# Performance work log

Measured on AMD Instinct MI355X. Metric: run time of the kernel, lower is better.

Reference implementation:

```python
import jax, jax.numpy as jnp
import numpy as np

NUM_HEADS = 8
EMBED = 512
HEAD_DIM = EMBED // NUM_HEADS
B, S = 4, 2048


def setup_inputs() -> dict:
    key = jax.random.key(0)
    ks = jax.random.split(key, 8)
    sc = 0.02
    return {
        "values": jax.random.normal(ks[0], (B, S, EMBED), dtype=jnp.float32),
        "keys": jax.random.normal(ks[1], (B, S, EMBED), dtype=jnp.float32),
        "query": jax.random.normal(ks[2], (B, S, EMBED), dtype=jnp.float32),
        "Wv": jax.random.normal(ks[3], (HEAD_DIM, HEAD_DIM), dtype=jnp.float32) * sc,
        "Wk": jax.random.normal(ks[4], (HEAD_DIM, HEAD_DIM), dtype=jnp.float32) * sc,
        "Wq": jax.random.normal(ks[5], (HEAD_DIM, HEAD_DIM), dtype=jnp.float32) * sc,
        "Wo": jax.random.normal(ks[6], (EMBED, EMBED), dtype=jnp.float32) * sc,
        "bo": jnp.zeros((EMBED,), dtype=jnp.float32),
    }


def reference(values, keys, query, Wv, Wk, Wq, Wo, bo):
    b, s, _ = query.shape
    # split heads: [B, S, H, D]
    v = values.reshape(b, s, NUM_HEADS, HEAD_DIM)
    k = keys.reshape(b, s, NUM_HEADS, HEAD_DIM)
    q = query.reshape(b, s, NUM_HEADS, HEAD_DIM)
    # per-head linear (nn.Linear: x @ W.T), weights shared across heads
    v = jnp.einsum("bshd,ed->bshe", v, Wv)
    k = jnp.einsum("bshd,ed->bshe", k, Wk)
    q = jnp.einsum("bshd,ed->bshe", q, Wq)
    # energy: [B, H, Q, K]
    energy = jnp.einsum("bqhd,bkhd->bhqk", q, k)
    # NOTE: original scales by sqrt(embed_size), not sqrt(head_dim)
    attn = jax.nn.softmax(energy / jnp.sqrt(jnp.float32(EMBED)), axis=-1)
    out = jnp.einsum("bhqk,bkhd->bqhd", attn, v).reshape(b, s, EMBED)
    return out @ Wo.T + bo
```

## Files before the change

kernel.cpp:

```cpp
#include <hip/hip_runtime.h>

#define H 8
#define D 64
#define E 512
#define BATCH 4
#define SEQ 2048

typedef __bf16 bf16v8 __attribute__((ext_vector_type(8)));
typedef float f32v4 __attribute__((ext_vector_type(4)));
typedef unsigned int u32v4 __attribute__((ext_vector_type(4)));
typedef unsigned short u16v4 __attribute__((ext_vector_type(4)));

#define MFMA16(a,b,c) __builtin_amdgcn_mfma_f32_16x16x32_bf16(a,b,c,0,0,0)

#define AS1 __attribute__((address_space(1)))
#define AS3 __attribute__((address_space(3)))
#define GLDS16(g, l) __builtin_amdgcn_global_load_lds((const AS1 void*)(g), (AS3 void*)(l), 16, 0, 0)

static __device__ __forceinline__ unsigned short f2bf(float f) {
  unsigned u = __builtin_bit_cast(unsigned, f);
  u += 0x7fffu + ((u >> 16) & 1u);
  return (unsigned short)(u >> 16);
}

static __device__ __forceinline__ float exp2_hw(float x) {
#if __has_builtin(__builtin_amdgcn_exp2f)
  return __builtin_amdgcn_exp2f(x);
#else
  return exp2f(x);
#endif
}

static __device__ __forceinline__ bf16v8 lds16(const char* p) {
  return __builtin_bit_cast(bf16v8, *(const u32v4*)p);
}

static __device__ __forceinline__ unsigned cvtpk(float a, float b) {
  unsigned r;
  asm("v_cvt_pk_bf16_f32 %0, %1, %2" : "=v"(r) : "v"(a), "v"(b));
  return r;
}

__global__ void prep_all(const float* __restrict__ Wo, const float* __restrict__ Wv,
                         const float* __restrict__ Wq, const float* __restrict__ Wk,
                         const float* __restrict__ v, const float* __restrict__ keys,
                         unsigned short* __restrict__ Wo2, unsigned short* __restrict__ MT,
                         unsigned short* __restrict__ vT, unsigned short* __restrict__ kb) {
  __shared__ float tile[64][65];
  int bx = blockIdx.x;
  int t = threadIdx.x;
  if (bx < 1024) {
    int i = bx * 256 + t;
    int n = i >> 9, c = i & 511;
    int h = c >> 6, d = c & 63;
    float acc = 0.f;
    for (int e = 0; e < 64; ++e) acc += Wo[n*512 + h*64 + e] * Wv[e*64 + d];
    Wo2[n*512 + c] = f2bf(acc);
  } else if (bx < 1040) {
    int i = (bx - 1024) * 256 + t;
    int d2 = i >> 6, d1 = i & 63;
    float acc = 0.f;
    for (int e = 0; e < 64; ++e) acc += Wq[e*64 + d1] * Wk[e*64 + d2];
    MT[d2*64 + d1] = f2bf(acc * 0.04419417382415922f);
  } else {
    int flat = bx - 1040;
    int bh = flat >> 5, sc = flat & 31;
    int b = bh >> 3, h = bh & 7;
    {
      const float* kp = keys + (size_t)flat * 4096;
      unsigned short* ko = kb + (size_t)flat * 4096;
      #pragma unroll
      for (int i = 0; i < 4; ++i) {
        f32v4 x = *(const f32v4*)(kp + (i*256 + t)*4);
        u16v4 o = { f2bf(x[0]), f2bf(x[1]), f2bf(x[2]), f2bf(x[3]) };
        *(u16v4*)(ko + (i*256 + t)*4) = o;
      }
    }
    #pragma unroll
    for (int i = 0; i < 4; ++i) {
      int idx = i*256 + t; int si = idx >> 4, fc = (idx & 15)*4;
      *(f32v4*)&tile[si][fc] =
          *(const f32v4*)(v + (size_t)(b*SEQ + sc*64 + si)*E + h*64 + fc);
    }
    __syncthreads();
    #pragma unroll
    for (int i = 0; i < 4; ++i) {
      int idx = i*256 + t; int d = idx >> 4, s4 = (idx & 15)*4;
      u16v4 o = { f2bf(tile[s4+0][d]), f2bf(tile[s4+1][d]),
                  f2bf(tile[s4+2][d]), f2bf(tile[s4+3][d]) };
      *(u16v4*)(vT + (size_t)(bh*64 + d)*SEQ + sc*64 + s4) = o;
    }
  }
}

__global__ __launch_bounds__(256, 4) void attn(const float* __restrict__ query,
                                               const unsigned short* __restrict__ MT,
                                               const unsigned short* __restrict__ kb,
                                               const unsigned short* __restrict__ vT,
                                               unsigned short* __restrict__ ao) {
  __shared__ __align__(16) char lds[40960];
  int orig = blockIdx.x;
  int workid = (orig & 7) * 128 + (orig >> 3);
  int bh = workid >> 5, qt = workid & 31;
  int b = bh >> 3, h = bh & 7;
  int tid = threadIdx.x, w = tid >> 6, lane = tid & 63, hi = lane >> 4, lo = lane & 15;
  int b4 = hi & 1;

  const unsigned short* kbase = kb + (size_t)(b*SEQ)*E + h*64;
  const unsigned short* vbase = vT + (size_t)bh*64*SEQ;
  int srow = tid >> 3, scc = tid & 7;

  #pragma unroll
  for (int i = 0; i < 2; ++i) {
    int row = i*32 + srow;
    int sc = scc ^ (row & 7);
    GLDS16(kbase + (size_t)row*E + sc*8,   lds        + i*4096 + w*1024);
    GLDS16(vbase + (size_t)row*SEQ + sc*8, lds + 8192 + i*4096 + w*1024);
  }
  {
    char* xl = lds + 32768;
    #pragma unroll
    for (int i = 0; i < 4; ++i) {
      int c = i*256 + tid;
      int row = c >> 4, cc = c & 15;
      f32v4 xv = *(const f32v4*)(query + (size_t)(b*SEQ + qt*64 + row)*E + h*64 + cc*4);
      u16v4 o = { f2bf(xv[0]), f2bf(xv[1]), f2bf(xv[2]), f2bf(xv[3]) };
      int off = row*128 + ((((cc >> 1) ^ (row & 7))) << 4) + (cc & 1)*8;
      *(u16v4*)(xl + off) = o;
    }
  }
  __syncthreads();

  bf16v8 qa[2];
  {
    const char* xl = lds + 32768;
    bf16v8 qrf[2];
    #pragma unroll
    for (int kk = 0; kk < 2; ++kk) {
      int row = w*16 + lo;
      qrf[kk] = lds16(xl + row*128 + (((kk*4 + hi) ^ (row & 7)) << 4));
    }
    f32v4 qacc[4] = {};
    #pragma unroll
    for (int kk = 0; kk < 2; ++kk)
      #pragma unroll
      for (int nt = 0; nt < 4; ++nt) {
        bf16v8 mtf = *(const bf16v8*)(MT + (nt*16 + lo)*64 + kk*32 + hi*8);
        qacc[nt] = MFMA16(mtf, qrf[kk], qacc[nt]);
      }
    unsigned qv[2][2][2];
    #pragma unroll
    for (int nt = 0; nt < 4; ++nt) {
      qv[nt >> 1][nt & 1][0] = cvtpk(qacc[nt][0], qacc[nt][1]);
      qv[nt >> 1][nt & 1][1] = cvtpk(qacc[nt][2], qacc[nt][3]);
    }
    #pragma unroll
    for (int nt1 = 0; nt1 < 2; ++nt1)
      #pragma unroll
      for (int s = 0; s < 2; ++s)
        asm("v_permlane32_swap_b32 %0, %1"
            : "+v"(qv[nt1][0][s]), "+v"(qv[nt1][1][s]));
    #pragma unroll
    for (int nt1 = 0; nt1 < 2; ++nt1)
      #pragma unroll
      for (int s = 0; s < 2; ++s) {
        int sent = b4 ? (int)qv[nt1][0][s] : (int)qv[nt1][1][s];
        unsigned recv = (unsigned)__shfl_xor(sent, 16);
        unsigned n0 = b4 ? recv : qv[nt1][0][s];
        unsigned n1 = b4 ? qv[nt1][1][s] : recv;
        qv[nt1][0][s] = n0;
        qv[nt1][1][s] = n1;
      }
    #pragma unroll
    for (int kk = 0; kk < 2; ++kk) {
      u32v4 c0 = { qv[kk][0][0], qv[kk][0][1], qv[kk][1][0], qv[kk][1][1] };
      qa[kk] = __builtin_bit_cast(bf16v8, c0);
    }
  }

  f32v4 oacc[4] = {};
  float lsum = 0.f;

  for (int kt = 0; kt < 32; ++kt) {
    const char* klc = lds + (kt & 1)*16384;
    const char* vlc = klc + 8192;
    if (kt < 31) {
      char* kln = lds + ((kt & 1) ^ 1)*16384;
      #pragma unroll
      for (int i = 0; i < 2; ++i) {
        int row = i*32 + srow;
        int sc = scc ^ (row & 7);
        GLDS16(kbase + (size_t)((kt+1)*64 + row)*E + sc*8, kln        + i*4096 + w*1024);
        GLDS16(vbase + (size_t)row*SEQ + (kt+1)*64 + sc*8, kln + 8192 + i*4096 + w*1024);
      }
    }
    f32v4 sacc[4] = {};
    __builtin_amdgcn_s_setprio(1);
    #pragma unroll
    for (int nt = 0; nt < 4; ++nt)
      #pragma unroll
      for (int kk = 0; kk < 2; ++kk) {
        int row = nt*16 + lo;
        bf16v8 kf = lds16(klc + row*128 + (((kk*4 + hi) ^ (row & 7)) << 4));
        sacc[nt] = MFMA16(kf, qa[kk], sacc[nt]);
      }
    __builtin_amdgcn_s_setprio(0);
    unsigned wv[2][2][2];
    #pragma unroll
    for (int nt = 0; nt < 4; ++nt) {
      float p0 = exp2_hw(sacc[nt][0] * 1.4426950408889634f);
      float p1 = exp2_hw(sacc[nt][1] * 1.4426950408889634f);
      float p2 = exp2_hw(sacc[nt][2] * 1.4426950408889634f);
      float p3 = exp2_hw(sacc[nt][3] * 1.4426950408889634f);
      lsum += (p0 + p1) + (p2 + p3);
      wv[nt >> 1][nt & 1][0] = cvtpk(p0, p1);
      wv[nt >> 1][nt & 1][1] = cvtpk(p2, p3);
    }
    #pragma unroll
    for (int nt1 = 0; nt1 < 2; ++nt1)
      #pragma unroll
      for (int s = 0; s < 2; ++s)
        asm("v_permlane32_swap_b32 %0, %1"
            : "+v"(wv[nt1][0][s]), "+v"(wv[nt1][1][s]));
    #pragma unroll
    for (int nt1 = 0; nt1 < 2; ++nt1)
      #pragma unroll
      for (int s = 0; s < 2; ++s) {
        int sent = b4 ? (int)wv[nt1][0][s] : (int)wv[nt1][1][s];
        unsigned recv = (unsigned)__shfl_xor(sent, 16);
        unsigned n0 = b4 ? recv : wv[nt1][0][s];
        unsigned n1 = b4 ? wv[nt1][1][s] : recv;
        wv[nt1][0][s] = n0;
        wv[nt1][1][s] = n1;
      }
    __builtin_amdgcn_s_setprio(1);
    #pragma unroll
    for (int ks = 0; ks < 2; ++ks) {
      u32v4 c0 = { wv[ks][0][0], wv[ks][0][1], wv[ks][1][0], wv[ks][1][1] };
      bf16v8 pb = __builtin_bit_cast(bf16v8, c0);
      #pragma unroll
      for (int dt = 0; dt < 4; ++dt) {
        int row = dt*16 + lo;
        bf16v8 vf = lds16(vlc + row*128 + (((ks*4 + hi) ^ (row & 7)) << 4));
        oacc[dt] = MFMA16(vf, pb, oacc[dt]);
      }
    }
    __builtin_amdgcn_s_setprio(0);
    __syncthreads();
  }
  lsum += __shfl_xor(lsum, 16);
  lsum += __shfl_xor(lsum, 32);
  lsum = __builtin_amdgcn_rcpf(lsum);
  {
    int tok = b*SEQ + qt*64 + w*16 + lo;
    #pragma unroll
    for (int dt = 0; dt < 4; ++dt) {
      u16v4 o = { f2bf(oacc[dt][0] * lsum), f2bf(oacc[dt][1] * lsum),
                  f2bf(oacc[dt][2] * lsum), f2bf(oacc[dt][3] * lsum) };
      *(u16v4*)(ao + (size_t)tok*E + h*64 + dt*16 + 4*hi) = o;
    }
  }
}

__global__ __launch_bounds__(256, 2) void final_gemm(const unsigned short* __restrict__ ao,
                                                     const unsigned short* __restrict__ wo2,
                                                     const float* __restrict__ bo,
                                                     float* __restrict__ out) {
  __shared__ __align__(16) char lds[49152];
  int m0 = blockIdx.x * 64, n0 = blockIdx.y * 128;
  int tid = threadIdx.x, w = tid >> 6, lane = tid & 63, hi = lane >> 4, lo = lane & 15;
  int wm = (w >> 1) * 32, wn = (w & 1) * 64;
  int srow = tid >> 3, scc = tid & 7;
  f32v4 acc[2][4] = {};
  #pragma unroll
  for (int i = 0; i < 2; ++i) {
    int row = i*32 + srow;
    int sc = scc ^ (row & 7);
    GLDS16(ao + (size_t)(m0 + row)*E + sc*8, lds + i*4096 + w*1024);
  }
  #pragma unroll
  for (int i = 0; i < 4; ++i) {
    int row = i*32 + srow;
    int sc = scc ^ (row & 7);
    GLDS16(wo2 + (size_t)(n0 + row)*E + sc*8, lds + 8192 + i*4096 + w*1024);
  }
  __syncthreads();
  for (int kt = 0; kt < 8; ++kt) {
    const char* al = lds + (kt & 1)*24576;
    const char* bl = al + 8192;
    if (kt < 7) {
      char* an = lds + ((kt & 1) ^ 1)*24576;
      #pragma unroll
      for (int i = 0; i < 2; ++i) {
        int row = i*32 + srow;
        int sc = scc ^ (row & 7);
        GLDS16(ao + (size_t)(m0 + row)*E + (kt+1)*64 + sc*8, an + i*4096 + w*1024);
      }
      #pragma unroll
      for (int i = 0; i < 4; ++i) {
        int row = i*32 + srow;
        int sc = scc ^ (row & 7);
        GLDS16(wo2 + (size_t)(n0 + row)*E + (kt+1)*64 + sc*8, an + 8192 + i*4096 + w*1024);
      }
    }
    __builtin_amdgcn_s_setprio(1);
    #pragma unroll
    for (int kk = 0; kk < 2; ++kk) {
      bf16v8 af[2], bfv[4];
      #pragma unroll
      for (int mt = 0; mt < 2; ++mt) {
        int row = wm + mt*16 + lo;
        af[mt] = lds16(al + row*128 + (((kk*4 + hi) ^ (row & 7)) << 4));
      }
      #pragma unroll
      for (int nt = 0; nt < 4; ++nt) {
        int row = wn + nt*16 + lo;
        bfv[nt] = lds16(bl + row*128 + (((kk*4 + hi) ^ (row & 7)) << 4));
      }
      #pragma unroll
      for (int mt = 0; mt < 2; ++mt)
        #pragma unroll
        for (int nt = 0; nt < 4; ++nt)
          acc[mt][nt] = MFMA16(af[mt], bfv[nt], acc[mt][nt]);
    }
    __builtin_amdgcn_s_setprio(0);
    __syncthreads();
  }
  #pragma unroll
  for (int nt = 0; nt < 4; ++nt) {
    float bias = bo[n0 + wn + nt*16 + lo];
    #pragma unroll
    for (int mt = 0; mt < 2; ++mt)
      #pragma unroll
      for (int r = 0; r < 4; ++r)
        out[(size_t)(m0 + wm + mt*16 + 4*hi + r)*E + n0 + wn + nt*16 + lo] =
            acc[mt][nt][r] + bias;
  }
}

extern "C" void kernel_launch(void* const* d_in, const int* in_sizes, int n_in,
                              void* d_out, int out_size, void* d_ws, size_t ws_size,
                              hipStream_t stream) {
  const float* values = (const float*)d_in[0];
  const float* keys   = (const float*)d_in[1];
  const float* query  = (const float*)d_in[2];
  const float* Wv     = (const float*)d_in[3];
  const float* Wk     = (const float*)d_in[4];
  const float* Wq     = (const float*)d_in[5];
  const float* Wo     = (const float*)d_in[6];
  const float* bo     = (const float*)d_in[7];
  float* out = (float*)d_out;
  char* ws = (char*)d_ws;

  unsigned short* MT  = (unsigned short*)(ws);
  unsigned short* Wo2 = (unsigned short*)(ws + 8192);
  unsigned short* kb  = (unsigned short*)(ws + (1u  << 20));
  unsigned short* vT  = (unsigned short*)(ws + (9u  << 20));
  unsigned short* ao  = (unsigned short*)(ws + (17u << 20));

  prep_all  <<<2064, 256, 0, stream>>>(Wo, Wv, Wq, Wk, values, keys, Wo2, MT, vT, kb);
  attn      <<<1024, 256, 0, stream>>>(query, MT, kb, vT, ao);
  final_gemm<<<dim3(128, 4), 256, 0, stream>>>(ao, Wo2, bo, out);
}
```

Baseline: 166.9 us.

## Process 128 queries per attention block to reuse K/V tiles across two M-tiles

Each attention workgroup now handles 128 query rows (two 16-row tiles per wave) instead of 64, halving the grid and reusing each K/V LDS tile and fragment load for twice the MFMA work. The log2(e) factor is folded into the precomputed MT scale so the per-element multiply before exp2 is dropped. The shfl_xor-based lane exchange is replaced with a v_permlane16_swap instruction. Occupancy drops (launch bounds 2, larger LDS, more registers) and there are only 512 blocks, which may underfill the GPU.

```diff
diff --git a/kernel.cpp b/kernel.cpp
--- a/kernel.cpp
+++ b/kernel.cpp
@@ -61,7 +61,7 @@
     int d2 = i >> 6, d1 = i & 63;
     float acc = 0.f;
     for (int e = 0; e < 64; ++e) acc += Wq[e*64 + d1] * Wk[e*64 + d2];
-    MT[d2*64 + d1] = f2bf(acc * 0.04419417382415922f);
+    MT[d2*64 + d1] = f2bf(acc * 0.06375872536061346f);
   } else {
     int flat = bx - 1040;
     int bh = flat >> 5, sc = flat & 31;
@@ -93,18 +93,17 @@
   }
 }
 
-__global__ __launch_bounds__(256, 4) void attn(const float* __restrict__ query,
+__global__ __launch_bounds__(256, 2) void attn(const float* __restrict__ query,
                                                const unsigned short* __restrict__ MT,
                                                const unsigned short* __restrict__ kb,
                                                const unsigned short* __restrict__ vT,
                                                unsigned short* __restrict__ ao) {
-  __shared__ __align__(16) char lds[40960];
+  __shared__ __align__(16) char lds[49152];
   int orig = blockIdx.x;
-  int workid = (orig & 7) * 128 + (orig >> 3);
-  int bh = workid >> 5, qt = workid & 31;
+  int workid = (orig & 7) * 64 + (orig >> 3);
+  int bh = workid >> 4, qt = workid & 15;
   int b = bh >> 3, h = bh & 7;
   int tid = threadIdx.x, w = tid >> 6, lane = tid & 63, hi = lane >> 4, lo = lane & 15;
-  int b4 = hi & 1;
 
   const unsigned short* kbase = kb + (size_t)(b*SEQ)*E + h*64;
   const unsigned short* vbase = vT + (size_t)bh*64*SEQ;
@@ -120,10 +119,10 @@
   {
     char* xl = lds + 32768;
     #pragma unroll
-    for (int i = 0; i < 4; ++i) {
+    for (int i = 0; i < 8; ++i) {
       int c = i*256 + tid;
       int row = c >> 4, cc = c & 15;
-      f32v4 xv = *(const f32v4*)(query + (size_t)(b*SEQ + qt*64 + row)*E + h*64 + cc*4);
+      f32v4 xv = *(const f32v4*)(query + (size_t)(b*SEQ + qt*128 + row)*E + h*64 + cc*4);
       u16v4 o = { f2bf(xv[0]), f2bf(xv[1]), f2bf(xv[2]), f2bf(xv[3]) };
       int off = row*128 + ((((cc >> 1) ^ (row & 7))) << 4) + (cc & 1)*8;
       *(u16v4*)(xl + off) = o;
@@ -131,55 +130,53 @@
   }
   __syncthreads();
 
-  bf16v8 qa[2];
+  bf16v8 qa[2][2];
   {
     const char* xl = lds + 32768;
-    bf16v8 qrf[2];
-    #pragma unroll
-    for (int kk = 0; kk < 2; ++kk) {
-      int row = w*16 + lo;
-      qrf[kk] = lds16(xl + row*128 + (((kk*4 + hi) ^ (row & 7)) << 4));
-    }
-    f32v4 qacc[4] = {};
+    bf16v8 qrf[2][2];
+    #pragma unroll
+    for (int m = 0; m < 2; ++m)
+      #pragma unroll
+      for (int kk = 0; kk < 2; ++kk) {
+        int row = w*32 + m*16 + lo;
+        qrf[m][kk] = lds16(xl + row*128 + (((kk*4 + hi) ^ (row & 7)) << 4));
+      }
+    f32v4 qacc[2][4] = {};
     #pragma unroll
     for (int kk = 0; kk < 2; ++kk)
       #pragma unroll
       for (int nt = 0; nt < 4; ++nt) {
         bf16v8 mtf = *(const bf16v8*)(MT + (nt*16 + lo)*64 + kk*32 + hi*8);
-        qacc[nt] = MFMA16(mtf, qrf[kk], qacc[nt]);
-      }
-    unsigned qv[2][2][2];
-    #pragma unroll
-    for (int nt = 0; nt < 4; ++nt) {
-      qv[nt >> 1][nt & 1][0] = cvtpk(qacc[nt][0], qacc[nt][1]);
-      qv[nt >> 1][nt & 1][1] = cvtpk(qacc[nt][2], qacc[nt][3]);
-    }
-    #pragma unroll
-    for (int nt1 = 0; nt1 < 2; ++nt1)
-      #pragma unroll
-      for (int s = 0; s < 2; ++s)
-        asm("v_permlane32_swap_b32 %0, %1"
-            : "+v"(qv[nt1][0][s]), "+v"(qv[nt1][1][s]));
-    #pragma unroll
-    for (int nt1 = 0; nt1 < 2; ++nt1)
-      #pragma unroll
-      for (int s = 0; s < 2; ++s) {
-        int sent = b4 ? (int)qv[nt1][0][s] : (int)qv[nt1][1][s];
-        unsigned recv = (unsigned)__shfl_xor(sent, 16);
-        unsigned n0 = b4 ? recv : qv[nt1][0][s];
-        unsigned n1 = b4 ? qv[nt1][1][s] : recv;
-        qv[nt1][0][s] = n0;
-        qv[nt1][1][s] = n1;
-      }
-    #pragma unroll
-    for (int kk = 0; kk < 2; ++kk) {
-      u32v4 c0 = { qv[kk][0][0], qv[kk][0][1], qv[kk][1][0], qv[kk][1][1] };
-      qa[kk] = __builtin_bit_cast(bf16v8, c0);
-    }
-  }
-
-  f32v4 oacc[4] = {};
-  float lsum = 0.f;
+        qacc[0][nt] = MFMA16(mtf, qrf[0][kk], qacc[0][nt]);
+        qacc[1][nt] = MFMA16(mtf, qrf[1][kk], qacc[1][nt]);
+      }
+    #pragma unroll
+    for (int m = 0; m < 2; ++m) {
+      unsigned qv[2][2][2];
+      #pragma unroll
+      for (int nt = 0; nt < 4; ++nt) {
+        qv[nt >> 1][nt & 1][0] = cvtpk(qacc[m][nt][0], qacc[m][nt][1]);
+        qv[nt >> 1][nt & 1][1] = cvtpk(qacc[m][nt][2], qacc[m][nt][3]);
+      }
+      #pragma unroll
+      for (int nt1 = 0; nt1 < 2; ++nt1)
+        #pragma unroll
+        for (int s = 0; s < 2; ++s) {
+          asm("v_permlane32_swap_b32 %0, %1"
+              : "+v"(qv[nt1][0][s]), "+v"(qv[nt1][1][s]));
+          asm("v_permlane16_swap_b32 %0, %1"
+              : "+v"(qv[nt1][0][s]), "+v"(qv[nt1][1][s]));
+        }
+      #pragma unroll
+      for (int kk = 0; kk < 2; ++kk) {
+        u32v4 c0 = { qv[kk][0][0], qv[kk][0][1], qv[kk][1][0], qv[kk][1][1] };
+        qa[m][kk] = __builtin_bit_cast(bf16v8, c0);
+      }
+    }
+  }
+
+  f32v4 oacc[2][4] = {};
+  float lsum[2] = {0.f, 0.f};
 
   for (int kt = 0; kt < 32; ++kt) {
     const char* klc = lds + (kt & 1)*16384;
@@ -194,7 +191,7 @@
         GLDS16(vbase + (size_t)row*SEQ + (kt+1)*64 + sc*8, kln + 8192 + i*4096 + w*1024);
       }
     }
-    f32v4 sacc[4] = {};
+    f32v4 sacc[2][4] = {};
     __builtin_amdgcn_s_setprio(1);
     #pragma unroll
     for (int nt = 0; nt < 4; ++nt)
@@ -202,61 +199,65 @@
       for (int kk = 0; kk < 2; ++kk) {
         int row = nt*16 + lo;
         bf16v8 kf = lds16(klc + row*128 + (((kk*4 + hi) ^ (row & 7)) << 4));
-        sacc[nt] = MFMA16(kf, qa[kk], sacc[nt]);
+        sacc[0][nt] = MFMA16(kf, qa[0][kk], sacc[0][nt]);
+        sacc[1][nt] = MFMA16(kf, qa[1][kk], sacc[1][nt]);
       }
     __builtin_amdgcn_s_setprio(0);
-    unsigned wv[2][2][2];
-    #pragma unroll
-    for (int nt = 0; nt < 4; ++nt) {
-      float p0 = exp2_hw(sacc[nt][0] * 1.4426950408889634f);
-      float p1 = exp2_hw(sacc[nt][1] * 1.4426950408889634f);
-      float p2 = exp2_hw(sacc[nt][2] * 1.4426950408889634f);
-      float p3 = exp2_hw(sacc[nt][3] * 1.4426950408889634f);
-      lsum += (p0 + p1) + (p2 + p3);
-      wv[nt >> 1][nt & 1][0] = cvtpk(p0, p1);
-      wv[nt >> 1][nt & 1][1] = cvtpk(p2, p3);
-    }
-    #pragma unroll
-    for (int nt1 = 0; nt1 < 2; ++nt1)
-      #pragma unroll
-      for (int s = 0; s < 2; ++s)
-        asm("v_permlane32_swap_b32 %0, %1"
-            : "+v"(wv[nt1][0][s]), "+v"(wv[nt1][1][s]));
-    #pragma unroll
-    for (int nt1 = 0; nt1 < 2; ++nt1)
-      #pragma unroll
-      for (int s = 0; s < 2; ++s) {
-        int sent = b4 ? (int)wv[nt1][0][s] : (int)wv[nt1][1][s];
-        unsigned recv = (unsigned)__shfl_xor(sent, 16);
-        unsigned n0 = b4 ? recv : wv[nt1][0][s];
-        unsigned n1 = b4 ? wv[nt1][1][s] : recv;
-        wv[nt1][0][s] = n0;
-        wv[nt1][1][s] = n1;
-      }
+    unsigned wv[2][2][2][2];
+    #pragma unroll
+    for (int m = 0; m < 2; ++m)
+      #pragma unroll
+      for (int nt = 0; nt < 4; ++nt) {
+        float p0 = exp2_hw(sacc[m][nt][0]);
+        float p1 = exp2_hw(sacc[m][nt][1]);
+        float p2 = exp2_hw(sacc[m][nt][2]);
+        float p3 = exp2_hw(sacc[m][nt][3]);
+        lsum[m] += (p0 + p1) + (p2 + p3);
+        wv[m][nt >> 1][nt & 1][0] = cvtpk(p0, p1);
+        wv[m][nt >> 1][nt & 1][1] = cvtpk(p2, p3);
+      }
+    #pragma unroll
+    for (int m = 0; m < 2; ++m)
+      #pragma unroll
+      for (int nt1 = 0; nt1 < 2; ++nt1)
+        #pragma unroll
+        for (int s = 0; s < 2; ++s) {
+          asm("v_permlane32_swap_b32 %0, %1"
+              : "+v"(wv[m][nt1][0][s]), "+v"(wv[m][nt1][1][s]));
+          asm("v_permlane16_swap_b32 %0, %1"
+              : "+v"(wv[m][nt1][0][s]), "+v"(wv[m][nt1][1][s]));
+        }
     __builtin_amdgcn_s_setprio(1);
     #pragma unroll
     for (int ks = 0; ks < 2; ++ks) {
-      u32v4 c0 = { wv[ks][0][0], wv[ks][0][1], wv[ks][1][0], wv[ks][1][1] };
-      bf16v8 pb = __builtin_bit_cast(bf16v8, c0);
+      u32v4 c0 = { wv[0][ks][0][0], wv[0][ks][0][1], wv[0][ks][1][0], wv[0][ks][1][1] };
+      u32v4 c1 = { wv[1][ks][0][0], wv[1][ks][0][1], wv[1][ks][1][0], wv[1][ks][1][1] };
+      bf16v8 pb0 = __builtin_bit_cast(bf16v8, c0);
+      bf16v8 pb1 = __builtin_bit_cast(bf16v8, c1);
       #pragma unroll
       for (int dt = 0; dt < 4; ++dt) {
         int row = dt*16 + lo;
         bf16v8 vf = lds16(vlc + row*128 + (((ks*4 + hi) ^ (row & 7)) << 4));
-        oacc[dt] = MFMA16(vf, pb, oacc[dt]);
+        oacc[0][dt] = MFMA16(vf, pb0, oacc[0][dt]);
+        oacc[1][dt] = MFMA16(vf, pb1, oacc[1][dt]);
       }
     }
     __builtin_amdgcn_s_setprio(0);
     __syncthreads();
   }
-  lsum += __shfl_xor(lsum, 16);
-  lsum += __shfl_xor(lsum, 32);
-  lsum = __builtin_amdgcn_rcpf(lsum);
-  {
-    int tok = b*SEQ + qt*64 + w*16 + lo;
+  #pragma unroll
+  for (int m = 0; m < 2; ++m) {
+    lsum[m] += __shfl_xor(lsum[m], 16);
+    lsum[m] += __shfl_xor(lsum[m], 32);
+    lsum[m] = __builtin_amdgcn_rcpf(lsum[m]);
+  }
+  #pragma unroll
+  for (int m = 0; m < 2; ++m) {
+    int tok = b*SEQ + qt*128 + w*32 + m*16 + lo;
     #pragma unroll
     for (int dt = 0; dt < 4; ++dt) {
-      u16v4 o = { f2bf(oacc[dt][0] * lsum), f2bf(oacc[dt][1] * lsum),
-                  f2bf(oacc[dt][2] * lsum), f2bf(oacc[dt][3] * lsum) };
+      u16v4 o = { f2bf(oacc[m][dt][0] * lsum[m]), f2bf(oacc[m][dt][1] * lsum[m]),
+                  f2bf(oacc[m][dt][2] * lsum[m]), f2bf(oacc[m][dt][3] * lsum[m]) };
       *(u16v4*)(ao + (size_t)tok*E + h*64 + dt*16 + 4*hi) = o;
     }
   }
@@ -359,6 +360,6 @@
   unsigned short* ao  = (unsigned short*)(ws + (17u << 20));
 
   prep_all  <<<2064, 256, 0, stream>>>(Wo, Wv, Wq, Wk, values, keys, Wo2, MT, vT, kb);
-  attn      <<<1024, 256, 0, stream>>>(query, MT, kb, vT, ao);
+  attn      <<<512,  256, 0, stream>>>(query, MT, kb, vT, ao);
   final_gemm<<<dim3(128, 4), 256, 0, stream>>>(ao, Wo2, bo, out);
 }
```

Measured after the change: 156.2 us. 1.07x faster.
